# Kernel tuning notes

Hardware: AMD Instinct MI355X
Metric: run time of the kernel (lower is better)

Reference implementation:

```python
import jax, jax.numpy as jnp
import numpy as np

N_DISEASES = 8192
N_MIRNAS = 16384
N_TOTAL = N_DISEASES + N_MIRNAS
D = 256
B = 65536
K = 50
EPS = 1e-8


def setup_inputs() -> dict:
    key = jax.random.key(0)
    k1, k2, k3, k4, k5, k6 = jax.random.split(key, 6)
    h = jax.random.normal(k1, (N_TOTAL, D), dtype=jnp.float32)
    emb = jax.random.normal(k2, (N_TOTAL, D), dtype=jnp.float32)
    src_init = jax.random.normal(k3, (B, D), dtype=jnp.float32)
    dst_init = jax.random.normal(k4, (B, D), dtype=jnp.float32)
    diseases = jax.random.randint(k5, (B,), 0, N_DISEASES, dtype=jnp.int32)
    mirnas = jax.random.randint(k6, (B,), N_DISEASES, N_TOTAL, dtype=jnp.int32)
    return {"h": h, "emb": emb, "src_init": src_init, "dst_init": dst_init,
            "diseases": diseases, "mirnas": mirnas}


def _cos(a, b):
    # cosine similarity along the last axis, eps-clamped like torch's F.cosine_similarity
    na = jnp.maximum(jnp.linalg.norm(a, axis=-1), EPS)
    nb = jnp.maximum(jnp.linalg.norm(b, axis=-1), EPS)
    return jnp.sum(a * b, axis=-1) / (na * nb)


def _pair_contrastive(pos_sim, neg_sim):
    # -log(exp(pos) / (exp(pos) + exp(neg))) = logaddexp(0, neg - pos)
    return jnp.mean(jnp.logaddexp(jnp.float32(0.0), neg_sim - pos_sim))


def _knn_feature_update(features, k):
    # [N, N] dense similarity, top-(k+1), drop self, gather + mean
    sim = features @ features.T                      # [N, N]
    _, idx = jax.lax.top_k(sim, k + 1)               # [N, k+1]
    idx = idx[:, 1:]                                 # drop self-match
    nbr = features[idx]                              # [N, k, D]
    return jnp.mean(nbr, axis=1)                     # [N, D]


def _knn_contrastive(feat_a, feat_b):
    center_a = jnp.mean(feat_a, axis=0)
    center_b = jnp.mean(feat_b, axis=0)
    sa_a = _cos(feat_a, center_a[None, :])
    sb_a = _cos(feat_a, center_b[None, :])
    loss_a = _pair_contrastive(sa_a, sb_a)
    sb_b = _cos(feat_b, center_b[None, :])
    sa_b = _cos(feat_b, center_a[None, :])
    loss_b = _pair_contrastive(sb_b, sa_b)
    return (loss_a + loss_b) * jnp.float32(0.5)


def reference(h, emb, src_init, dst_init, diseases, mirnas):
    h_d = h[diseases]                                # [B, D]
    h_m = h[mirnas]                                  # [B, D]
    pos_sim = _cos(h_d, src_init)
    neg_sim = _cos(h_d, dst_init)
    contrastive_loss = _pair_contrastive(pos_sim, neg_sim)

    upd_d = _knn_feature_update(emb[:N_DISEASES], K)
    upd_m = _knn_feature_update(emb[N_DISEASES:], K)
    feature_contrastive_loss = _knn_contrastive(upd_d, upd_m)

    # interactionPredictor modeled as sigmoid dot-product scorer
    scores = jax.nn.sigmoid(jnp.sum(h_d * h_m, axis=-1))  # [B]
    return scores, contrastive_loss, feature_contrastive_loss
```

## Files before the change

### kernel.cpp

```cpp
#include <hip/hip_runtime.h>
#include <math.h>

#define NDIS 8192
#define NMIR 16384
#define NTOT 24576
#define DIMD 256
#define BPAIR 65536
#define KSEL 50
#define EPSF 1e-8f
#define SW 2048
#define CBC 32
#define NCH (SW / CBC)
#define CAPD 80
#define CAPM 40
#define PSTR 320
#define ZD 2.066f
#define ZM 2.418f
#define ZFD 0.9035f
#define ZFM 1.331f
#define PPB 2048

typedef __attribute__((ext_vector_type(8))) short bf16x8;
typedef __attribute__((ext_vector_type(4))) float f32x4;
typedef unsigned long long ull;

__device__ __forceinline__ float wredsum(float v) {
#pragma unroll
  for (int off = 1; off < 64; off <<= 1) v += __shfl_xor(v, off, 64);
  return v;
}

__device__ __forceinline__ int wredsumi(int v) {
#pragma unroll
  for (int off = 1; off < 64; off <<= 1) v += __shfl_xor(v, off, 64);
  return v;
}

__device__ __forceinline__ float softplusf(float x) {
  return fmaxf(x, 0.0f) + log1pf(expf(-fabsf(x)));
}

__device__ __forceinline__ float dot4f(const float4 a, const float4 b) {
  return a.x * b.x + a.y * b.y + a.z * b.z + a.w * b.w;
}

__device__ __forceinline__ unsigned short f2bf(float f) {
  unsigned u = __float_as_uint(f);
  unsigned r = (u + 0x7fffu + ((u >> 16) & 1u)) >> 16;
  return (unsigned short)r;
}

__device__ __forceinline__ float b2f(unsigned short x) {
  return __uint_as_float((unsigned)x << 16);
}

__device__ __forceinline__ unsigned ordu(float f) {
  unsigned u = __float_as_uint(f);
  return (u & 0x80000000u) ? ~u : (u | 0x80000000u);
}

__global__ __launch_bounds__(256) void convert_kernel(
    const float* __restrict__ in, unsigned short* __restrict__ out) {
  const int i = (blockIdx.x * 256 + threadIdx.x) * 4;
  const float4 v = *(const float4*)(in + i);
  ushort4 o;
  o.x = f2bf(v.x); o.y = f2bf(v.y); o.z = f2bf(v.z); o.w = f2bf(v.w);
  *(ushort4*)(out + i) = o;
}

__global__ __launch_bounds__(256) void colsum_kernel(
    const unsigned short* __restrict__ embb, float* __restrict__ colpart) {
  const int d = threadIdx.x;
  const int r0 = blockIdx.x * 256;
  float s = 0.0f;
  for (int i = 0; i < 256; ++i) s += b2f(embb[(size_t)(r0 + i) * DIMD + d]);
  colpart[blockIdx.x * DIMD + d] = s;
}

__global__ __launch_bounds__(256) void colmean_kernel(
    const float* __restrict__ colpart, float* __restrict__ colmean) {
  const int g = blockIdx.x;
  const int d = threadIdx.x;
  const int b0 = g ? 32 : 0, b1 = g ? 96 : 32;
  const float N = g ? (float)NMIR : (float)NDIS;
  float s = 0.0f;
  for (int b = b0; b < b1; ++b) s += colpart[b * DIMD + d];
  colmean[g * DIMD + d] = s / N;
}

__global__ __launch_bounds__(256) void tau_kernel(
    const unsigned short* __restrict__ embb, const float* __restrict__ colmean,
    float* __restrict__ tau, float2* __restrict__ musig,
    unsigned* __restrict__ cnts, unsigned* __restrict__ flags) {
  const int lane = threadIdx.x & 63;
  const int widx = threadIdx.x >> 6;
  const int r0 = blockIdx.x * 256 + widx * 64;
  for (int rr = 0; rr < 64; ++rr) {
    const int row = r0 + rr;
    const bool ism = row >= NDIS;
    const float4 cm = ((const float4*)(colmean + (ism ? DIMD : 0)))[lane];
    const ushort4 u = ((const ushort4*)(embb + (size_t)row * DIMD))[lane];
    const float fx = b2f(u.x), fy = b2f(u.y), fz = b2f(u.z), fw = b2f(u.w);
    float dot = fx * cm.x + fy * cm.y + fz * cm.z + fw * cm.w;
    float nsq = fx * fx + fy * fy + fz * fz + fw * fw;
    dot = wredsum(dot);
    nsq = wredsum(nsq);
    const float sig = sqrtf(nsq);
    if (lane == 0) {
      tau[row] = dot + (ism ? ZM : ZD) * sig;
      musig[row] = make_float2(dot, sig);
      flags[row] = 0u;
    }
    if (lane < 8) cnts[row * 8 + lane] = 0u;
  }
}

__global__ __launch_bounds__(256) void pair_kernel(
    const float* __restrict__ h, const float* __restrict__ srci,
    const float* __restrict__ dsti, const int* __restrict__ dis,
    const int* __restrict__ mir, float* __restrict__ scores,
    float* __restrict__ pairpart) {
  const int lane = threadIdx.x & 63;
  const int widx = threadIdx.x >> 6;
  const int gw = blockIdx.x * 4 + widx;
  float lsum = 0.0f;
  for (int b = gw; b < BPAIR; b += PPB * 4) {
    const int d = dis[b];
    const int m = mir[b];
    const float4 a4 = ((const float4*)(h + (size_t)d * DIMD))[lane];
    const float4 m4 = ((const float4*)(h + (size_t)m * DIMD))[lane];
    const float4 s4 = ((const float4*)(srci + (size_t)b * DIMD))[lane];
    const float4 t4 = ((const float4*)(dsti + (size_t)b * DIMD))[lane];
    float aa = dot4f(a4, a4);
    float ss = dot4f(s4, s4);
    float tt = dot4f(t4, t4);
    float as = dot4f(a4, s4);
    float at = dot4f(a4, t4);
    float am = dot4f(a4, m4);
    aa = wredsum(aa); ss = wredsum(ss); tt = wredsum(tt);
    as = wredsum(as); at = wredsum(at); am = wredsum(am);
    const float ra = fmaxf(sqrtf(aa), EPSF);
    const float pos = as / (ra * fmaxf(sqrtf(ss), EPSF));
    const float neg = at / (ra * fmaxf(sqrtf(tt), EPSF));
    lsum += softplusf(neg - pos);
    if (lane == 0) scores[b] = 1.0f / (1.0f + expf(-am));
  }
  __shared__ float wsum[4];
  if (lane == 0) wsum[widx] = lsum;
  __syncthreads();
  if (threadIdx.x == 0)
    pairpart[blockIdx.x] = (wsum[0] + wsum[1]) + (wsum[2] + wsum[3]);
}

__global__ __launch_bounds__(256, 3) void knn_kernel(
    const unsigned short* __restrict__ embb, const float* __restrict__ tau,
    unsigned* __restrict__ part, unsigned* __restrict__ cnts,
    unsigned* __restrict__ flags) {
  __shared__ char lds[3][CBC * 512];

  const int tid = threadIdx.x;
  const int lane = tid & 63;
  const int widx = tid >> 6;
  const int q4 = lane >> 4;
  const int l15 = lane & 15;
  const int sh16 = q4 * 16;
  const unsigned lmask = (1u << l15) - 1u;

  const int bid = blockIdx.x;
  const bool ism = bid < 1024;
  const int rt = ism ? (bid >> 3) : ((bid - 1024) >> 2);
  const int strip = ism ? (bid & 7) : ((bid - 1024) & 3);
  const int cap = ism ? CAPM : CAPD;
  const int gbase = ism ? NDIS : 0;
  const unsigned short* fb = embb + (size_t)gbase * DIMD;

  const int rowbase = rt * 128 + widx * 32;
  const int colstart = strip * SW;
  const char* gb = (const char*)fb;

  bf16x8 afr[2][8];
#pragma unroll
  for (int rg = 0; rg < 2; ++rg) {
    const int arow = rowbase + rg * 16 + l15;
    const char* ab = (const char*)fb + (size_t)arow * 512 + q4 * 16;
#pragma unroll
    for (int kk = 0; kk < 8; ++kk)
      afr[rg][kk] = *(const bf16x8*)(ab + (size_t)kk * 64);
  }

  float tau8[2][4];
  unsigned offb[2];
  int cnt8[2][4];
#pragma unroll
  for (int rg = 0; rg < 2; ++rg) {
    const int db = rowbase + rg * 16 + q4 * 4;
    offb[rg] = (unsigned)(gbase + db) * PSTR + strip * cap;
#pragma unroll
    for (int j = 0; j < 4; ++j) {
      tau8[rg][j] = tau[gbase + db + j];
      cnt8[rg][j] = 0;
    }
  }

  auto stage = [&](char* dst, int cb0n) {
#pragma unroll
    for (int it = 0; it < 4; ++it) {
      const int m = widx * 4 + it;
      const int col = m * 2 + (lane >> 5);
      const int qq = (lane & 31) * 16;
      const int koff = qq ^ ((col & 7) << 4);
      const char* src = gb + (size_t)(colstart + cb0n + col) * 512 + koff;
      __builtin_amdgcn_global_load_lds(
          (const __attribute__((address_space(1))) void*)src,
          (__attribute__((address_space(3))) void*)(dst + m * 1024), 16, 0, 0);
    }
  };

  char* b0 = lds[0];
  char* b1 = lds[1];
  char* b2 = lds[2];
  stage(b0, 0);
  stage(b1, CBC);
  for (int ch = 0; ch < NCH; ++ch) {
    if (ch < NCH - 1)
      asm volatile("s_waitcnt vmcnt(4)" ::: "memory");
    else
      asm volatile("s_waitcnt vmcnt(0)" ::: "memory");
    __builtin_amdgcn_sched_barrier(0);
    __builtin_amdgcn_s_barrier();
    __builtin_amdgcn_sched_barrier(0);
    if (ch + 2 < NCH) stage(b2, (ch + 2) * CBC);

    const char* bch = b0;
    const int cb0 = ch * CBC;
    f32x4 acc[2][2];
#pragma unroll
    for (int rg = 0; rg < 2; ++rg)
#pragma unroll
      for (int t = 0; t < 2; ++t) acc[rg][t] = (f32x4){0.f, 0.f, 0.f, 0.f};

#pragma unroll
    for (int t = 0; t < 2; ++t) {
      const int col = t * 16 + l15;
      const char* bbase = bch + (size_t)col * 512;
      const int xr = (col & 7) << 4;
#pragma unroll
      for (int kk = 0; kk < 8; ++kk) {
        const int koff = (kk * 64 + (q4 * 16)) ^ xr;
        const bf16x8 b = *(const bf16x8*)(bbase + koff);
        acc[0][t] = __builtin_amdgcn_mfma_f32_16x16x32_bf16(afr[0][kk], b,
                                                            acc[0][t], 0, 0, 0);
        acc[1][t] = __builtin_amdgcn_mfma_f32_16x16x32_bf16(afr[1][kk], b,
                                                            acc[1][t], 0, 0, 0);
      }
    }

#pragma unroll
    for (int t = 0; t < 2; ++t) {
      const int colb = colstart + cb0 + t * 16;
      const unsigned kc = (unsigned)(16383 - (colb + l15));
#pragma unroll
      for (int rg = 0; rg < 2; ++rg) {
        const bool dchr = (colb == rowbase + rg * 16);
#pragma unroll
        for (int j = 0; j < 4; ++j) {
          const float v = acc[rg][t][j];
          bool ok = v > tau8[rg][j];
          if (dchr) ok = ok && (l15 != (q4 * 4 + j));
          const ull m = __ballot(ok);
          if (m) {
            const unsigned m16 = (unsigned)(m >> sh16) & 0xFFFFu;
            const int rank = __popc(m16 & lmask);
            const int slot = cnt8[rg][j] + rank;
            if (ok && slot < cap)
              part[offb[rg] + (unsigned)(j * PSTR) + slot] =
                  ((ordu(v) >> 14) << 14) | kc;
            cnt8[rg][j] += __popc(m16);
          }
        }
      }
    }

    char* tp = b0; b0 = b1; b1 = b2; b2 = tp;
  }

#pragma unroll
  for (int rg = 0; rg < 2; ++rg) {
#pragma unroll
    for (int j = 0; j < 4; ++j) {
      if (l15 == 0) {
        const int growg = gbase + rowbase + rg * 16 + q4 * 4 + j;
        const int c = cnt8[rg][j];
        cnts[growg * 8 + strip] = (unsigned)(c < cap ? c : cap);
        if (c > cap) flags[growg] = 1u;
      }
    }
  }
}

__global__ __launch_bounds__(256) void fallback_kernel(
    const unsigned short* __restrict__ embb, const float2* __restrict__ musig,
    unsigned* __restrict__ part, unsigned* __restrict__ cnts,
    const unsigned* __restrict__ flags, unsigned* __restrict__ fbbuf) {
  __shared__ unsigned short frow[4][DIMD];
  const int lane = threadIdx.x & 63;
  const int widx = threadIdx.x >> 6;
  const int wid = blockIdx.x * 4 + widx;
  const ull bel = (1ull << lane) - 1ull;

  for (int row = wid * 96; row < wid * 96 + 96; ++row) {
    unsigned tot = 0;
    for (int s = 0; s < 8; ++s) tot += cnts[row * 8 + s];
    if (!(flags[row] || tot < KSEL)) continue;

    const bool ism = row >= NDIS;
    const int lrow = ism ? row - NDIS : row;
    const int Ng = ism ? NMIR : NDIS;
    const unsigned short* fb = embb + (ism ? (size_t)NDIS * DIMD : 0);
    const float2 ms = musig[row];
    const float tp = ms.x + (ism ? ZFM : ZFD) * ms.y;

    ((ushort4*)frow[widx])[lane] =
        ((const ushort4*)(fb + (size_t)lrow * DIMD))[lane];

    unsigned* fk = fbbuf + (size_t)wid * 4096;
    int fc = 0;
    for (int cb = 0; cb < Ng; cb += 64) {
      const int col = cb + lane;
      float s = 0.0f;
      for (int d0 = 0; d0 < DIMD; d0 += 4) {
        const ushort4 uc = *(const ushort4*)(fb + (size_t)col * DIMD + d0);
        const ushort4 ur = *(const ushort4*)(&frow[widx][d0]);
        s += b2f(uc.x) * b2f(ur.x) + b2f(uc.y) * b2f(ur.y) +
             b2f(uc.z) * b2f(ur.z) + b2f(uc.w) * b2f(ur.w);
      }
      const bool a = (s > tp) && (col != lrow);
      const ull m = __ballot(a);
      const int sl = fc + __popcll(m & bel);
      if (a && sl < 4096) fk[sl] = ((ordu(s) >> 14) << 14) | (16383u - col);
      fc += __popcll(m);
    }
    if (fc > 4096) fc = 4096;

    unsigned lo = 0u, hi = 0xFFFFFFFFu;
    for (int it = 0; it < 32; ++it) {
      const unsigned mid = lo + ((hi - lo) >> 1);
      int c = 0;
      for (int i = lane; i < fc; i += 64) c += (fk[i] > mid) ? 1 : 0;
      c = wredsumi(c);
      if (c >= KSEL) lo = mid; else hi = mid;
    }
    int wc = 0;
    for (int base = 0; base < fc; base += 64) {
      const int i = base + lane;
      const bool w = (i < fc) && (fk[i] > lo);
      const ull m = __ballot(w);
      const int pos = wc + __popcll(m & bel);
      if (w) part[(size_t)row * PSTR + pos] = fk[i];
      wc += __popcll(m);
    }
    if (lane < 8) cnts[row * 8 + lane] = (lane == 0) ? KSEL : 0u;
  }
}

__global__ __launch_bounds__(256) void merge_kernel(
    const unsigned short* __restrict__ embb, const unsigned* __restrict__ part,
    const unsigned* __restrict__ cnts, float* __restrict__ upd_d,
    float* __restrict__ upd_m) {
  __shared__ unsigned kb[4][PSTR];
  const int lane = threadIdx.x & 63;
  const int widx = threadIdx.x >> 6;
  const int row = blockIdx.x * 4 + widx;
  const bool ism = row >= NDIS;
  const int lrow = ism ? row - NDIS : row;
  const unsigned short* fe = embb + (ism ? (size_t)NDIS * DIMD : 0);
  float* upd =
      (ism ? upd_m + (size_t)lrow * DIMD : upd_d + (size_t)lrow * DIMD);
  const int ns = ism ? 8 : 4;
  const int cap = ism ? CAPM : CAPD;
  const ull bel = (1ull << lane) - 1ull;

  int T = 0;
  for (int s = 0; s < ns; ++s) {
    const int c = (int)cnts[row * 8 + s];
    for (int i = lane; i < c; i += 64)
      kb[widx][T + i] = part[(size_t)row * PSTR + s * cap + i];
    T += c;
  }
  unsigned k[5];
#pragma unroll
  for (int i = 0; i < 5; ++i) {
    const int idx = i * 64 + lane;
    k[i] = (idx < T) ? kb[widx][idx] : 0u;
  }

  unsigned lo = 0u, hi = 0xFFFFFFFFu;
  for (int it = 0; it < 32; ++it) {
    const unsigned mid = lo + ((hi - lo) >> 1);
    int c = 0;
#pragma unroll
    for (int i = 0; i < 5; ++i) c += __popcll(__ballot(k[i] > mid));
    if (c >= KSEL) lo = mid; else hi = mid;
  }
  int wc = 0;
#pragma unroll
  for (int i = 0; i < 5; ++i) {
    const bool w = k[i] > lo;
    const ull m = __ballot(w);
    const int pos = wc + __popcll(m & bel);
    if (w) kb[widx][pos] = 16383u - (k[i] & 16383u);
    wc += __popcll(m);
  }

  float ax = 0.f, ay = 0.f, az = 0.f, aw = 0.f;
#pragma unroll 10
  for (int t = 0; t < KSEL; ++t) {
    const int col = (int)kb[widx][t];
    const ushort4 u = ((const ushort4*)(fe + (size_t)col * DIMD))[lane];
    ax += b2f(u.x); ay += b2f(u.y); az += b2f(u.z); aw += b2f(u.w);
  }
  const float inv = 1.0f / (float)KSEL;
  float4 o;
  o.x = ax * inv; o.y = ay * inv; o.z = az * inv; o.w = aw * inv;
  ((float4*)upd)[lane] = o;
}

__global__ __launch_bounds__(256) void center_partial(
    const float* __restrict__ upd, const int N, float* __restrict__ part) {
  const int c = threadIdx.x;
  const int rows_per = N >> 7;
  const int r0 = blockIdx.x * rows_per;
  float s = 0.0f;
  for (int i = 0; i < rows_per; ++i) s += upd[(size_t)(r0 + i) * DIMD + c];
  part[blockIdx.x * DIMD + c] = s;
}

__global__ __launch_bounds__(256) void center_final(
    const float* __restrict__ part, const int N, float* __restrict__ center,
    float* __restrict__ cnorm) {
  const int c = threadIdx.x;
  float s = 0.0f;
  for (int b = 0; b < 128; ++b) s += part[b * DIMD + c];
  s /= (float)N;
  center[c] = s;
  __shared__ float red[256];
  red[c] = s * s;
  __syncthreads();
  for (int off = 128; off > 0; off >>= 1) {
    if (c < off) red[c] += red[c + off];
    __syncthreads();
  }
  if (c == 0) cnorm[0] = sqrtf(red[0]);
}

__global__ __launch_bounds__(256) void knn_loss(
    const float* __restrict__ upd, const int N,
    const float* __restrict__ centers, const float* __restrict__ cnorms,
    const int group, float* __restrict__ part) {
  const int lane = threadIdx.x & 63;
  const int widx = threadIdx.x >> 6;
  const int gw = blockIdx.x * 4 + widx;
  const float4 ca = ((const float4*)centers)[lane];
  const float4 cbv = ((const float4*)(centers + DIMD))[lane];
  const float na = fmaxf(cnorms[0], EPSF);
  const float nb = fmaxf(cnorms[1], EPSF);
  float lsum = 0.0f;
  for (int r = gw; r < N; r += 1024) {
    const float4 u = ((const float4*)(upd + (size_t)r * DIMD))[lane];
    float uu = dot4f(u, u);
    float uca = dot4f(u, ca);
    float ucb = dot4f(u, cbv);
    uu = wredsum(uu); uca = wredsum(uca); ucb = wredsum(ucb);
    const float nu = fmaxf(sqrtf(uu), EPSF);
    const float sa = uca / (nu * na);
    const float sb = ucb / (nu * nb);
    const float x = (group == 0) ? (sb - sa) : (sa - sb);
    lsum += softplusf(x);
  }
  __shared__ float wsum[4];
  if (lane == 0) wsum[widx] = lsum;
  __syncthreads();
  if (threadIdx.x == 0)
    part[blockIdx.x] = (wsum[0] + wsum[1]) + (wsum[2] + wsum[3]);
}

__global__ __launch_bounds__(256) void finalize_kernel(
    const float* __restrict__ pairpart, const float* __restrict__ lpa,
    const float* __restrict__ lpb, float* __restrict__ out) {
  __shared__ float red[256];
  const int t = threadIdx.x;

  float s = 0.0f;
  for (int i = t; i < PPB; i += 256) s += pairpart[i];
  red[t] = s;
  __syncthreads();
  for (int off = 128; off > 0; off >>= 1) {
    if (t < off) red[t] += red[t + off];
    __syncthreads();
  }
  const float pairsum = red[0];
  __syncthreads();

  red[t] = lpa[t];
  __syncthreads();
  for (int off = 128; off > 0; off >>= 1) {
    if (t < off) red[t] += red[t + off];
    __syncthreads();
  }
  const float la = red[0];
  __syncthreads();

  red[t] = lpb[t];
  __syncthreads();
  for (int off = 128; off > 0; off >>= 1) {
    if (t < off) red[t] += red[t + off];
    __syncthreads();
  }
  const float lb = red[0];

  if (t == 0) {
    out[BPAIR] = pairsum / (float)BPAIR;
    out[BPAIR + 1] = 0.5f * (la / (float)NDIS + lb / (float)NMIR);
  }
}

extern "C" void kernel_launch(void* const* d_in, const int* in_sizes, int n_in,
                              void* d_out, int out_size, void* d_ws,
                              size_t ws_size, hipStream_t stream) {
  const float* h = (const float*)d_in[0];
  const float* emb = (const float*)d_in[1];
  const float* srci = (const float*)d_in[2];
  const float* dsti = (const float*)d_in[3];
  const int* dis = (const int*)d_in[4];
  const int* mir = (const int*)d_in[5];
  float* out = (float*)d_out;

  float* W = (float*)d_ws;
  float* upd_d = W;
  float* upd_m = upd_d + (size_t)NDIS * DIMD;
  float* pairpart = upd_m + (size_t)NMIR * DIMD;
  float* cpart_d = pairpart + PPB;
  float* cpart_m = cpart_d + 32768;
  float* centers = cpart_m + 32768;
  float* cnorms = centers + 512;
  float* lpa = cnorms + 64;
  float* lpb = lpa + 256;
  float* colpart = lpb + 256;
  float* colmean = colpart + 96 * DIMD;
  float* tau = colmean + 512;
  float2* musig = (float2*)(tau + NTOT);
  unsigned* flags = (unsigned*)(musig + NTOT);
  unsigned* cnts = flags + NTOT;
  unsigned short* embb = (unsigned short*)(cnts + NTOT * 8);
  unsigned* part = (unsigned*)(embb + (size_t)NTOT * DIMD);
  unsigned* fbbuf = part + (size_t)NTOT * PSTR;

  convert_kernel<<<(NTOT * DIMD) / 1024, 256, 0, stream>>>(emb, embb);
  colsum_kernel<<<96, 256, 0, stream>>>(embb, colpart);
  colmean_kernel<<<2, 256, 0, stream>>>(colpart, colmean);
  tau_kernel<<<96, 256, 0, stream>>>(embb, colmean, tau, musig, cnts, flags);
  pair_kernel<<<PPB, 256, 0, stream>>>(h, srci, dsti, dis, mir, out, pairpart);
  knn_kernel<<<1280, 256, 0, stream>>>(embb, tau, part, cnts, flags);
  fallback_kernel<<<64, 256, 0, stream>>>(embb, musig, part, cnts, flags,
                                          fbbuf);
  merge_kernel<<<NTOT / 4, 256, 0, stream>>>(embb, part, cnts, upd_d, upd_m);
  center_partial<<<128, 256, 0, stream>>>(upd_d, NDIS, cpart_d);
  center_partial<<<128, 256, 0, stream>>>(upd_m, NMIR, cpart_m);
  center_final<<<1, 256, 0, stream>>>(cpart_d, NDIS, centers, cnorms);
  center_final<<<1, 256, 0, stream>>>(cpart_m, NMIR, centers + DIMD,
                                      cnorms + 1);
  knn_loss<<<256, 256, 0, stream>>>(upd_d, NDIS, centers, cnorms, 0, lpa);
  knn_loss<<<256, 256, 0, stream>>>(upd_m, NMIR, centers, cnorms, 1, lpb);
  finalize_kernel<<<1, 256, 0, stream>>>(pairpart, lpa, lpb, out);
}
```

Measured before the change: 529.5 us.

## Fuse pair loss into kNN kernel, rebalance strips, merge small reduction launches

The pair cosine/score computation now runs as a tail phase of the kNN MFMA kernel instead of its own launch. The miRNA kNN work is split into 4 strips of 4096 columns rather than 8 of 2048, with a single candidate cap of 80. The grid shrinks to 768 blocks, which fits one wave at 3 blocks per CU. The colmean step is folded into tau_kernel, and the separate per-group center_partial, center_final and knn_loss launches each become one launch that covers both groups, cutting launch count and tail waves. In exchange, each miRNA block does a longer serial column sweep and keeps more candidates per strip, and the pair phase adds latency at the end of each kNN block.

```diff
diff --git a/kernel.cpp b/kernel.cpp
--- a/kernel.cpp
+++ b/kernel.cpp
@@ -8,17 +8,14 @@
 #define BPAIR 65536
 #define KSEL 50
 #define EPSF 1e-8f
-#define SW 2048
 #define CBC 32
-#define NCH (SW / CBC)
-#define CAPD 80
-#define CAPM 40
+#define CAP 80
 #define PSTR 320
 #define ZD 2.066f
 #define ZM 2.418f
 #define ZFD 0.9035f
 #define ZFM 1.331f
-#define PPB 2048
+#define NKB 768
 
 typedef __attribute__((ext_vector_type(8))) short bf16x8;
 typedef __attribute__((ext_vector_type(4))) float f32x4;
@@ -77,54 +74,196 @@
   colpart[blockIdx.x * DIMD + d] = s;
 }
 
-__global__ __launch_bounds__(256) void colmean_kernel(
-    const float* __restrict__ colpart, float* __restrict__ colmean) {
-  const int g = blockIdx.x;
-  const int d = threadIdx.x;
-  const int b0 = g ? 32 : 0, b1 = g ? 96 : 32;
-  const float N = g ? (float)NMIR : (float)NDIS;
-  float s = 0.0f;
-  for (int b = b0; b < b1; ++b) s += colpart[b * DIMD + d];
-  colmean[g * DIMD + d] = s / N;
-}
-
 __global__ __launch_bounds__(256) void tau_kernel(
-    const unsigned short* __restrict__ embb, const float* __restrict__ colmean,
+    const unsigned short* __restrict__ embb, const float* __restrict__ colpart,
     float* __restrict__ tau, float2* __restrict__ musig,
     unsigned* __restrict__ cnts, unsigned* __restrict__ flags) {
+  __shared__ float cm[DIMD];
   const int lane = threadIdx.x & 63;
   const int widx = threadIdx.x >> 6;
+  const bool bism = blockIdx.x >= 32;
+  {
+    const int b0 = bism ? 32 : 0, b1 = bism ? 96 : 32;
+    const float Ninv = 1.0f / (bism ? (float)NMIR : (float)NDIS);
+    float s = 0.0f;
+    for (int b = b0; b < b1; ++b) s += colpart[b * DIMD + threadIdx.x];
+    cm[threadIdx.x] = s * Ninv;
+  }
+  __syncthreads();
   const int r0 = blockIdx.x * 256 + widx * 64;
+  const float z = bism ? ZM : ZD;
   for (int rr = 0; rr < 64; ++rr) {
     const int row = r0 + rr;
-    const bool ism = row >= NDIS;
-    const float4 cm = ((const float4*)(colmean + (ism ? DIMD : 0)))[lane];
+    const float4 cmv = ((const float4*)cm)[lane];
     const ushort4 u = ((const ushort4*)(embb + (size_t)row * DIMD))[lane];
     const float fx = b2f(u.x), fy = b2f(u.y), fz = b2f(u.z), fw = b2f(u.w);
-    float dot = fx * cm.x + fy * cm.y + fz * cm.z + fw * cm.w;
+    float dot = fx * cmv.x + fy * cmv.y + fz * cmv.z + fw * cmv.w;
     float nsq = fx * fx + fy * fy + fz * fz + fw * fw;
     dot = wredsum(dot);
     nsq = wredsum(nsq);
     const float sig = sqrtf(nsq);
     if (lane == 0) {
-      tau[row] = dot + (ism ? ZM : ZD) * sig;
+      tau[row] = dot + z * sig;
       musig[row] = make_float2(dot, sig);
       flags[row] = 0u;
     }
-    if (lane < 8) cnts[row * 8 + lane] = 0u;
-  }
-}
-
-__global__ __launch_bounds__(256) void pair_kernel(
-    const float* __restrict__ h, const float* __restrict__ srci,
-    const float* __restrict__ dsti, const int* __restrict__ dis,
-    const int* __restrict__ mir, float* __restrict__ scores,
-    float* __restrict__ pairpart) {
-  const int lane = threadIdx.x & 63;
-  const int widx = threadIdx.x >> 6;
-  const int gw = blockIdx.x * 4 + widx;
+    if (lane < 4) cnts[row * 4 + lane] = 0u;
+  }
+}
+
+__global__ __launch_bounds__(256, 3) void knn_kernel(
+    const unsigned short* __restrict__ embb, const float* __restrict__ tau,
+    unsigned* __restrict__ part, unsigned* __restrict__ cnts,
+    unsigned* __restrict__ flags, const float* __restrict__ h,
+    const float* __restrict__ srci, const float* __restrict__ dsti,
+    const int* __restrict__ dis, const int* __restrict__ mir,
+    float* __restrict__ scores, float* __restrict__ pairpart) {
+  __shared__ char lds[3][CBC * 512];
+  __shared__ float wsum[4];
+
+  const int tid = threadIdx.x;
+  const int lane = tid & 63;
+  const int widx = tid >> 6;
+  const int q4 = lane >> 4;
+  const int l15 = lane & 15;
+  const int sh16 = q4 * 16;
+  const unsigned lmask = (1u << l15) - 1u;
+
+  const int bid = blockIdx.x;
+  const bool ism = bid < 512;
+  const int rt = ism ? (bid >> 2) : ((bid - 512) >> 2);
+  const int strip = ism ? (bid & 3) : ((bid - 512) & 3);
+  const int sw = ism ? 4096 : 2048;
+  const int nch = sw / CBC;
+  const int gbase = ism ? NDIS : 0;
+  const unsigned short* fb = embb + (size_t)gbase * DIMD;
+
+  const int rowbase = rt * 128 + widx * 32;
+  const int colstart = strip * sw;
+  const char* gb = (const char*)fb;
+
+  bf16x8 afr[2][8];
+#pragma unroll
+  for (int rg = 0; rg < 2; ++rg) {
+    const int arow = rowbase + rg * 16 + l15;
+    const char* ab = (const char*)fb + (size_t)arow * 512 + q4 * 16;
+#pragma unroll
+    for (int kk = 0; kk < 8; ++kk)
+      afr[rg][kk] = *(const bf16x8*)(ab + (size_t)kk * 64);
+  }
+
+  float tau8[2][4];
+  unsigned offb[2];
+  int cnt8[2][4];
+#pragma unroll
+  for (int rg = 0; rg < 2; ++rg) {
+    const int db = rowbase + rg * 16 + q4 * 4;
+    offb[rg] = (unsigned)(gbase + db) * PSTR + strip * CAP;
+#pragma unroll
+    for (int j = 0; j < 4; ++j) {
+      tau8[rg][j] = tau[gbase + db + j];
+      cnt8[rg][j] = 0;
+    }
+  }
+
+  auto stage = [&](char* dst, int cb0n) {
+#pragma unroll
+    for (int it = 0; it < 4; ++it) {
+      const int m = widx * 4 + it;
+      const int col = m * 2 + (lane >> 5);
+      const int qq = (lane & 31) * 16;
+      const int koff = qq ^ ((col & 7) << 4);
+      const char* src = gb + (size_t)(colstart + cb0n + col) * 512 + koff;
+      __builtin_amdgcn_global_load_lds(
+          (const __attribute__((address_space(1))) void*)src,
+          (__attribute__((address_space(3))) void*)(dst + m * 1024), 16, 0, 0);
+    }
+  };
+
+  char* b0 = lds[0];
+  char* b1 = lds[1];
+  char* b2 = lds[2];
+  stage(b0, 0);
+  stage(b1, CBC);
+  for (int ch = 0; ch < nch; ++ch) {
+    if (ch < nch - 1)
+      asm volatile("s_waitcnt vmcnt(4)" ::: "memory");
+    else
+      asm volatile("s_waitcnt vmcnt(0)" ::: "memory");
+    __builtin_amdgcn_sched_barrier(0);
+    __builtin_amdgcn_s_barrier();
+    __builtin_amdgcn_sched_barrier(0);
+    if (ch + 2 < nch) stage(b2, (ch + 2) * CBC);
+
+    const char* bch = b0;
+    const int cb0 = ch * CBC;
+    f32x4 acc[2][2];
+#pragma unroll
+    for (int rg = 0; rg < 2; ++rg)
+#pragma unroll
+      for (int t = 0; t < 2; ++t) acc[rg][t] = (f32x4){0.f, 0.f, 0.f, 0.f};
+
+#pragma unroll
+    for (int t = 0; t < 2; ++t) {
+      const int col = t * 16 + l15;
+      const char* bbase = bch + (size_t)col * 512;
+      const int xr = (col & 7) << 4;
+#pragma unroll
+      for (int kk = 0; kk < 8; ++kk) {
+        const int koff = (kk * 64 + (q4 * 16)) ^ xr;
+        const bf16x8 b = *(const bf16x8*)(bbase + koff);
+        acc[0][t] = __builtin_amdgcn_mfma_f32_16x16x32_bf16(afr[0][kk], b,
+                                                            acc[0][t], 0, 0, 0);
+        acc[1][t] = __builtin_amdgcn_mfma_f32_16x16x32_bf16(afr[1][kk], b,
+                                                            acc[1][t], 0, 0, 0);
+      }
+    }
+
+#pragma unroll
+    for (int t = 0; t < 2; ++t) {
+      const int colb = colstart + cb0 + t * 16;
+      const unsigned kc = (unsigned)(16383 - (colb + l15));
+#pragma unroll
+      for (int rg = 0; rg < 2; ++rg) {
+        const bool dchr = (colb == rowbase + rg * 16);
+#pragma unroll
+        for (int j = 0; j < 4; ++j) {
+          const float v = acc[rg][t][j];
+          bool ok = v > tau8[rg][j];
+          if (dchr) ok = ok && (l15 != (q4 * 4 + j));
+          const ull m = __ballot(ok);
+          if (m) {
+            const unsigned m16 = (unsigned)(m >> sh16) & 0xFFFFu;
+            const int rank = __popc(m16 & lmask);
+            const int slot = cnt8[rg][j] + rank;
+            if (ok && slot < CAP)
+              part[offb[rg] + (unsigned)(j * PSTR) + slot] =
+                  ((ordu(v) >> 14) << 14) | kc;
+            cnt8[rg][j] += __popc(m16);
+          }
+        }
+      }
+    }
+
+    char* tp = b0; b0 = b1; b1 = b2; b2 = tp;
+  }
+
+#pragma unroll
+  for (int rg = 0; rg < 2; ++rg) {
+#pragma unroll
+    for (int j = 0; j < 4; ++j) {
+      if (l15 == 0) {
+        const int growg = gbase + rowbase + rg * 16 + q4 * 4 + j;
+        const int c = cnt8[rg][j];
+        cnts[growg * 4 + strip] = (unsigned)(c < CAP ? c : CAP);
+        if (c > CAP) flags[growg] = 1u;
+      }
+    }
+  }
+
+  const int gw = bid * 4 + widx;
   float lsum = 0.0f;
-  for (int b = gw; b < BPAIR; b += PPB * 4) {
+  for (int b = gw; b < BPAIR; b += NKB * 4) {
     const int d = dis[b];
     const int m = mir[b];
     const float4 a4 = ((const float4*)(h + (size_t)d * DIMD))[lane];
@@ -145,157 +284,10 @@
     lsum += softplusf(neg - pos);
     if (lane == 0) scores[b] = 1.0f / (1.0f + expf(-am));
   }
-  __shared__ float wsum[4];
   if (lane == 0) wsum[widx] = lsum;
   __syncthreads();
-  if (threadIdx.x == 0)
-    pairpart[blockIdx.x] = (wsum[0] + wsum[1]) + (wsum[2] + wsum[3]);
-}
-
-__global__ __launch_bounds__(256, 3) void knn_kernel(
-    const unsigned short* __restrict__ embb, const float* __restrict__ tau,
-    unsigned* __restrict__ part, unsigned* __restrict__ cnts,
-    unsigned* __restrict__ flags) {
-  __shared__ char lds[3][CBC * 512];
-
-  const int tid = threadIdx.x;
-  const int lane = tid & 63;
-  const int widx = tid >> 6;
-  const int q4 = lane >> 4;
-  const int l15 = lane & 15;
-  const int sh16 = q4 * 16;
-  const unsigned lmask = (1u << l15) - 1u;
-
-  const int bid = blockIdx.x;
-  const bool ism = bid < 1024;
-  const int rt = ism ? (bid >> 3) : ((bid - 1024) >> 2);
-  const int strip = ism ? (bid & 7) : ((bid - 1024) & 3);
-  const int cap = ism ? CAPM : CAPD;
-  const int gbase = ism ? NDIS : 0;
-  const unsigned short* fb = embb + (size_t)gbase * DIMD;
-
-  const int rowbase = rt * 128 + widx * 32;
-  const int colstart = strip * SW;
-  const char* gb = (const char*)fb;
-
-  bf16x8 afr[2][8];
-#pragma unroll
-  for (int rg = 0; rg < 2; ++rg) {
-    const int arow = rowbase + rg * 16 + l15;
-    const char* ab = (const char*)fb + (size_t)arow * 512 + q4 * 16;
-#pragma unroll
-    for (int kk = 0; kk < 8; ++kk)
-      afr[rg][kk] = *(const bf16x8*)(ab + (size_t)kk * 64);
-  }
-
-  float tau8[2][4];
-  unsigned offb[2];
-  int cnt8[2][4];
-#pragma unroll
-  for (int rg = 0; rg < 2; ++rg) {
-    const int db = rowbase + rg * 16 + q4 * 4;
-    offb[rg] = (unsigned)(gbase + db) * PSTR + strip * cap;
-#pragma unroll
-    for (int j = 0; j < 4; ++j) {
-      tau8[rg][j] = tau[gbase + db + j];
-      cnt8[rg][j] = 0;
-    }
-  }
-
-  auto stage = [&](char* dst, int cb0n) {
-#pragma unroll
-    for (int it = 0; it < 4; ++it) {
-      const int m = widx * 4 + it;
-      const int col = m * 2 + (lane >> 5);
-      const int qq = (lane & 31) * 16;
-      const int koff = qq ^ ((col & 7) << 4);
-      const char* src = gb + (size_t)(colstart + cb0n + col) * 512 + koff;
-      __builtin_amdgcn_global_load_lds(
-          (const __attribute__((address_space(1))) void*)src,
-          (__attribute__((address_space(3))) void*)(dst + m * 1024), 16, 0, 0);
-    }
-  };
-
-  char* b0 = lds[0];
-  char* b1 = lds[1];
-  char* b2 = lds[2];
-  stage(b0, 0);
-  stage(b1, CBC);
-  for (int ch = 0; ch < NCH; ++ch) {
-    if (ch < NCH - 1)
-      asm volatile("s_waitcnt vmcnt(4)" ::: "memory");
-    else
-      asm volatile("s_waitcnt vmcnt(0)" ::: "memory");
-    __builtin_amdgcn_sched_barrier(0);
-    __builtin_amdgcn_s_barrier();
-    __builtin_amdgcn_sched_barrier(0);
-    if (ch + 2 < NCH) stage(b2, (ch + 2) * CBC);
-
-    const char* bch = b0;
-    const int cb0 = ch * CBC;
-    f32x4 acc[2][2];
-#pragma unroll
-    for (int rg = 0; rg < 2; ++rg)
-#pragma unroll
-      for (int t = 0; t < 2; ++t) acc[rg][t] = (f32x4){0.f, 0.f, 0.f, 0.f};
-
-#pragma unroll
-    for (int t = 0; t < 2; ++t) {
-      const int col = t * 16 + l15;
-      const char* bbase = bch + (size_t)col * 512;
-      const int xr = (col & 7) << 4;
-#pragma unroll
-      for (int kk = 0; kk < 8; ++kk) {
-        const int koff = (kk * 64 + (q4 * 16)) ^ xr;
-        const bf16x8 b = *(const bf16x8*)(bbase + koff);
-        acc[0][t] = __builtin_amdgcn_mfma_f32_16x16x32_bf16(afr[0][kk], b,
-                                                            acc[0][t], 0, 0, 0);
-        acc[1][t] = __builtin_amdgcn_mfma_f32_16x16x32_bf16(afr[1][kk], b,
-                                                            acc[1][t], 0, 0, 0);
-      }
-    }
-
-#pragma unroll
-    for (int t = 0; t < 2; ++t) {
-      const int colb = colstart + cb0 + t * 16;
-      const unsigned kc = (unsigned)(16383 - (colb + l15));
-#pragma unroll
-      for (int rg = 0; rg < 2; ++rg) {
-        const bool dchr = (colb == rowbase + rg * 16);
-#pragma unroll
-        for (int j = 0; j < 4; ++j) {
-          const float v = acc[rg][t][j];
-          bool ok = v > tau8[rg][j];
-          if (dchr) ok = ok && (l15 != (q4 * 4 + j));
-          const ull m = __ballot(ok);
-          if (m) {
-            const unsigned m16 = (unsigned)(m >> sh16) & 0xFFFFu;
-            const int rank = __popc(m16 & lmask);
-            const int slot = cnt8[rg][j] + rank;
-            if (ok && slot < cap)
-              part[offb[rg] + (unsigned)(j * PSTR) + slot] =
-                  ((ordu(v) >> 14) << 14) | kc;
-            cnt8[rg][j] += __popc(m16);
-          }
-        }
-      }
-    }
-
-    char* tp = b0; b0 = b1; b1 = b2; b2 = tp;
-  }
-
-#pragma unroll
-  for (int rg = 0; rg < 2; ++rg) {
-#pragma unroll
-    for (int j = 0; j < 4; ++j) {
-      if (l15 == 0) {
-        const int growg = gbase + rowbase + rg * 16 + q4 * 4 + j;
-        const int c = cnt8[rg][j];
-        cnts[growg * 8 + strip] = (unsigned)(c < cap ? c : cap);
-        if (c > cap) flags[growg] = 1u;
-      }
-    }
-  }
+  if (tid == 0)
+    pairpart[bid] = (wsum[0] + wsum[1]) + (wsum[2] + wsum[3]);
 }
 
 __global__ __launch_bounds__(256) void fallback_kernel(
@@ -310,7 +302,7 @@
 
   for (int row = wid * 96; row < wid * 96 + 96; ++row) {
     unsigned tot = 0;
-    for (int s = 0; s < 8; ++s) tot += cnts[row * 8 + s];
+    for (int s = 0; s < 4; ++s) tot += cnts[row * 4 + s];
     if (!(flags[row] || tot < KSEL)) continue;
 
     const bool ism = row >= NDIS;
@@ -359,7 +351,7 @@
       if (w) part[(size_t)row * PSTR + pos] = fk[i];
       wc += __popcll(m);
     }
-    if (lane < 8) cnts[row * 8 + lane] = (lane == 0) ? KSEL : 0u;
+    if (lane < 4) cnts[row * 4 + lane] = (lane == 0) ? KSEL : 0u;
   }
 }
 
@@ -376,15 +368,13 @@
   const unsigned short* fe = embb + (ism ? (size_t)NDIS * DIMD : 0);
   float* upd =
       (ism ? upd_m + (size_t)lrow * DIMD : upd_d + (size_t)lrow * DIMD);
-  const int ns = ism ? 8 : 4;
-  const int cap = ism ? CAPM : CAPD;
   const ull bel = (1ull << lane) - 1ull;
 
   int T = 0;
-  for (int s = 0; s < ns; ++s) {
-    const int c = (int)cnts[row * 8 + s];
+  for (int s = 0; s < 4; ++s) {
+    const int c = (int)cnts[row * 4 + s];
     for (int i = lane; i < c; i += 64)
-      kb[widx][T + i] = part[(size_t)row * PSTR + s * cap + i];
+      kb[widx][T + i] = part[(size_t)row * PSTR + s * CAP + i];
     T += c;
   }
   unsigned k[5];
@@ -426,23 +416,25 @@
 }
 
 __global__ __launch_bounds__(256) void center_partial(
-    const float* __restrict__ upd, const int N, float* __restrict__ part) {
+    const float* __restrict__ upd, float* __restrict__ part) {
   const int c = threadIdx.x;
-  const int rows_per = N >> 7;
-  const int r0 = blockIdx.x * rows_per;
+  const int r0 = blockIdx.x * 128;
   float s = 0.0f;
-  for (int i = 0; i < rows_per; ++i) s += upd[(size_t)(r0 + i) * DIMD + c];
+  for (int i = 0; i < 128; ++i) s += upd[(size_t)(r0 + i) * DIMD + c];
   part[blockIdx.x * DIMD + c] = s;
 }
 
 __global__ __launch_bounds__(256) void center_final(
-    const float* __restrict__ part, const int N, float* __restrict__ center,
+    const float* __restrict__ part, float* __restrict__ center,
     float* __restrict__ cnorm) {
+  const int g = blockIdx.x;
   const int c = threadIdx.x;
+  const int b0 = g ? 64 : 0, b1 = g ? 192 : 64;
+  const float N = g ? (float)NMIR : (float)NDIS;
   float s = 0.0f;
-  for (int b = 0; b < 128; ++b) s += part[b * DIMD + c];
-  s /= (float)N;
-  center[c] = s;
+  for (int b = b0; b < b1; ++b) s += part[b * DIMD + c];
+  s /= N;
+  center[g * DIMD + c] = s;
   __shared__ float red[256];
   red[c] = s * s;
   __syncthreads();
@@ -450,22 +442,28 @@
     if (c < off) red[c] += red[c + off];
     __syncthreads();
   }
-  if (c == 0) cnorm[0] = sqrtf(red[0]);
+  if (c == 0) cnorm[g] = sqrtf(red[0]);
 }
 
 __global__ __launch_bounds__(256) void knn_loss(
-    const float* __restrict__ upd, const int N,
+    const float* __restrict__ upd_d, const float* __restrict__ upd_m,
     const float* __restrict__ centers, const float* __restrict__ cnorms,
-    const int group, float* __restrict__ part) {
+    float* __restrict__ lpa, float* __restrict__ lpb) {
   const int lane = threadIdx.x & 63;
   const int widx = threadIdx.x >> 6;
-  const int gw = blockIdx.x * 4 + widx;
+  const int bid = blockIdx.x;
+  const bool ism = bid >= 128;
+  const int lb = ism ? bid - 128 : bid;
+  const int N = ism ? NMIR : NDIS;
+  const int nw = ism ? 1024 : 512;
+  const float* upd = ism ? upd_m : upd_d;
+  const int gw = lb * 4 + widx;
   const float4 ca = ((const float4*)centers)[lane];
   const float4 cbv = ((const float4*)(centers + DIMD))[lane];
   const float na = fmaxf(cnorms[0], EPSF);
   const float nb = fmaxf(cnorms[1], EPSF);
   float lsum = 0.0f;
-  for (int r = gw; r < N; r += 1024) {
+  for (int r = gw; r < N; r += nw) {
     const float4 u = ((const float4*)(upd + (size_t)r * DIMD))[lane];
     float uu = dot4f(u, u);
     float uca = dot4f(u, ca);
@@ -474,14 +472,16 @@
     const float nu = fmaxf(sqrtf(uu), EPSF);
     const float sa = uca / (nu * na);
     const float sb = ucb / (nu * nb);
-    const float x = (group == 0) ? (sb - sa) : (sa - sb);
+    const float x = ism ? (sa - sb) : (sb - sa);
     lsum += softplusf(x);
   }
   __shared__ float wsum[4];
   if (lane == 0) wsum[widx] = lsum;
   __syncthreads();
-  if (threadIdx.x == 0)
-    part[blockIdx.x] = (wsum[0] + wsum[1]) + (wsum[2] + wsum[3]);
+  if (threadIdx.x == 0) {
+    const float v = (wsum[0] + wsum[1]) + (wsum[2] + wsum[3]);
+    if (ism) lpb[lb] = v; else lpa[lb] = v;
+  }
 }
 
 __global__ __launch_bounds__(256) void finalize_kernel(
@@ -491,7 +491,7 @@
   const int t = threadIdx.x;
 
   float s = 0.0f;
-  for (int i = t; i < PPB; i += 256) s += pairpart[i];
+  for (int i = t; i < NKB; i += 256) s += pairpart[i];
   red[t] = s;
   __syncthreads();
   for (int off = 128; off > 0; off >>= 1) {
@@ -501,7 +501,7 @@
   const float pairsum = red[0];
   __syncthreads();
 
-  red[t] = lpa[t];
+  red[t] = (t < 128) ? lpa[t] : 0.0f;
   __syncthreads();
   for (int off = 128; off > 0; off >>= 1) {
     if (t < off) red[t] += red[t + off];
@@ -539,37 +539,30 @@
   float* upd_d = W;
   float* upd_m = upd_d + (size_t)NDIS * DIMD;
   float* pairpart = upd_m + (size_t)NMIR * DIMD;
-  float* cpart_d = pairpart + PPB;
-  float* cpart_m = cpart_d + 32768;
-  float* centers = cpart_m + 32768;
+  float* cpart = pairpart + 1024;
+  float* centers = cpart + 192 * DIMD;
   float* cnorms = centers + 512;
   float* lpa = cnorms + 64;
-  float* lpb = lpa + 256;
+  float* lpb = lpa + 128;
   float* colpart = lpb + 256;
-  float* colmean = colpart + 96 * DIMD;
-  float* tau = colmean + 512;
+  float* tau = colpart + 96 * DIMD;
   float2* musig = (float2*)(tau + NTOT);
   unsigned* flags = (unsigned*)(musig + NTOT);
   unsigned* cnts = flags + NTOT;
-  unsigned short* embb = (unsigned short*)(cnts + NTOT * 8);
+  unsigned short* embb = (unsigned short*)(cnts + NTOT * 4);
   unsigned* part = (unsigned*)(embb + (size_t)NTOT * DIMD);
   unsigned* fbbuf = part + (size_t)NTOT * PSTR;
 
   convert_kernel<<<(NTOT * DIMD) / 1024, 256, 0, stream>>>(emb, embb);
   colsum_kernel<<<96, 256, 0, stream>>>(embb, colpart);
-  colmean_kernel<<<2, 256, 0, stream>>>(colpart, colmean);
-  tau_kernel<<<96, 256, 0, stream>>>(embb, colmean, tau, musig, cnts, flags);
-  pair_kernel<<<PPB, 256, 0, stream>>>(h, srci, dsti, dis, mir, out, pairpart);
-  knn_kernel<<<1280, 256, 0, stream>>>(embb, tau, part, cnts, flags);
+  tau_kernel<<<96, 256, 0, stream>>>(embb, colpart, tau, musig, cnts, flags);
+  knn_kernel<<<NKB, 256, 0, stream>>>(embb, tau, part, cnts, flags, h, srci,
+                                      dsti, dis, mir, out, pairpart);
   fallback_kernel<<<64, 256, 0, stream>>>(embb, musig, part, cnts, flags,
                                           fbbuf);
   merge_kernel<<<NTOT / 4, 256, 0, stream>>>(embb, part, cnts, upd_d, upd_m);
-  center_partial<<<128, 256, 0, stream>>>(upd_d, NDIS, cpart_d);
-  center_partial<<<128, 256, 0, stream>>>(upd_m, NMIR, cpart_m);
-  center_final<<<1, 256, 0, stream>>>(cpart_d, NDIS, centers, cnorms);
-  center_final<<<1, 256, 0, stream>>>(cpart_m, NMIR, centers + DIMD,
-                                      cnorms + 1);
-  knn_loss<<<256, 256, 0, stream>>>(upd_d, NDIS, centers, cnorms, 0, lpa);
-  knn_loss<<<256, 256, 0, stream>>>(upd_m, NMIR, centers, cnorms, 1, lpb);
+  center_partial<<<192, 256, 0, stream>>>(upd_d, cpart);
+  center_final<<<2, 256, 0, stream>>>(cpart, centers, cnorms);
+  knn_loss<<<384, 256, 0, stream>>>(upd_d, upd_m, centers, cnorms, lpa, lpb);
   finalize_kernel<<<1, 256, 0, stream>>>(pairpart, lpa, lpb, out);
 }
```

Result: faster. 488.7 us (-7.7%).
